# Optimization experiments

Measured on AMD Instinct MI355X. Metric: run time of the kernel, lower is better.

The kernel has to match this reference:

```python
import jax, jax.numpy as jnp
import numpy as np


def setup_inputs() -> dict:
    key = jax.random.key(0)
    k1, k2 = jax.random.split(key)
    B, D, H, W, K = 16, 256, 32, 32, 8192
    x = jax.random.normal(k1, (B, D, H, W), dtype=jnp.float32)
    # init_tensor: uniform [0,1), L2-normalized along dim 0 (embedding_dim), * embedding_scale
    e = jax.random.uniform(k2, (D, K), dtype=jnp.float32)
    e_i_ts = e / jnp.linalg.norm(e, axis=0, keepdims=True)
    return {"x": x, "e_i_ts": e_i_ts}


def reference(x, e_i_ts):
    B, D = x.shape[0], x.shape[1]
    spatial = x.shape[2:]
    # permute [B, D, *spatial] -> [B, *spatial, D], flatten tokens
    perm = (0,) + tuple(range(2, x.ndim)) + (1,)
    flat_x = jnp.transpose(x, perm).reshape(-1, D)  # [N, D]
    distances = (
        jnp.sum(flat_x * flat_x, axis=1, keepdims=True)
        - 2.0 * (flat_x @ e_i_ts)
        + jnp.sum(e_i_ts * e_i_ts, axis=0, keepdims=True)
    )
    encoding_indices = jnp.argmin(distances, axis=1)  # [N]
    ind = encoding_indices.reshape((B,) + spatial)  # [B, *spatial]
    # gather codebook columns: e_i_ts.T[ind] -> [B, *spatial, D], back to channel-first
    quantized = jnp.take(e_i_ts.T, ind, axis=0)
    inv_perm = (0, x.ndim - 1) + tuple(range(1, x.ndim - 1))
    quantized_x = jnp.transpose(quantized, inv_perm)  # [B, D, *spatial]
    # straight-through estimator
    quantized_x_d = x + jax.lax.stop_gradient(quantized_x - x)
    return quantized_x_d, quantized_x, ind
```

## Files before the change

kernel.cpp:

```cpp
#include <hip/hip_runtime.h>
#include <hip/hip_bf16.h>
#include <hip/hip_fp16.h>


#define D_   256
#define HW_  1024
#define N_   16384
#define K_   8192
#define NB_  32
#define MARGIN 0.02f

#define OUT1_OFF 4194304
#define IND_OFF  8388608

typedef __attribute__((ext_vector_type(8))) _Float16 f16x8;
typedef __attribute__((ext_vector_type(4))) float f32x4;

__device__ __forceinline__ unsigned long long pack_dk(float dist, int k) {
    unsigned db = __float_as_uint(dist);
    unsigned mono = (db & 0x80000000u) ? ~db : (db | 0x80000000u);
    return ((unsigned long long)mono << 32) | (unsigned)k;
}

__device__ __forceinline__ void async_copy16(const void* g, void* l) {
    __builtin_amdgcn_global_load_lds(
        (const __attribute__((address_space(1))) void*)g,
        (__attribute__((address_space(3))) void*)l, 16, 0, 0);
}

__global__ __launch_bounds__(256)
void cnorm_kernel(const float* __restrict__ E, float* __restrict__ c,
                  int* __restrict__ counters) {
    if (blockIdx.x == 0 && threadIdx.x < 2) counters[threadIdx.x] = 0;
    __shared__ float part[8][32];
    const int tid = threadIdx.x;
    const int cl = tid & 31, q = tid >> 5;
    const int k = blockIdx.x * 32 + cl;
    float s = 0.f;
    #pragma unroll 8
    for (int d = q * 32; d < q * 32 + 32; ++d) {
        float v = E[(size_t)d * K_ + k];
        s = fmaf(v, v, s);
    }
    part[q][cl] = s;
    __syncthreads();
    if (tid < 32) {
        float t0 = (part[0][tid] + part[1][tid]) + (part[2][tid] + part[3][tid]);
        float t1 = (part[4][tid] + part[5][tid]) + (part[6][tid] + part[7][tid]);
        c[blockIdx.x * 32 + tid] = t0 + t1;
    }
}

__global__ __launch_bounds__(256)
void prep_x(const float* __restrict__ x, ushort* __restrict__ xf) {
    __shared__ float t[32][33];
    const int s0 = blockIdx.x * 32, d0 = blockIdx.y * 32, b = blockIdx.z;
    const int tid = threadIdx.x;
    #pragma unroll
    for (int j = 0; j < 4; ++j) {
        int i = tid + 256 * j; int dd = i >> 5, ss = i & 31;
        t[dd][ss] = x[(size_t)b * 262144 + (size_t)(d0 + dd) * 1024 + s0 + ss];
    }
    __syncthreads();
    #pragma unroll
    for (int j = 0; j < 4; ++j) {
        int i = tid + 256 * j; int ss = i >> 5, dd = i & 31;
        _Float16 h = (_Float16)t[dd][ss];
        size_t o = (size_t)(b * 1024 + s0 + ss) * D_ + d0 + dd;
        xf[o] = *(ushort*)&h;
    }
}

__global__ __launch_bounds__(256)
void prep_e(const float* __restrict__ E, ushort* __restrict__ ef) {
    __shared__ float t[32][33];
    const int k0 = blockIdx.x * 32, d0 = blockIdx.y * 32;
    const int tid = threadIdx.x;
    #pragma unroll
    for (int j = 0; j < 4; ++j) {
        int i = tid + 256 * j; int dd = i >> 5, kk = i & 31;
        t[dd][kk] = E[(size_t)(d0 + dd) * K_ + k0 + kk];
    }
    __syncthreads();
    #pragma unroll
    for (int j = 0; j < 4; ++j) {
        int i = tid + 256 * j; int kk = i >> 5, dd = i & 31;
        _Float16 h = (_Float16)t[dd][kk];
        ef[(size_t)(k0 + kk) * D_ + d0 + dd] = *(ushort*)&h;
    }
}

__global__ __launch_bounds__(256, 3)
void mfma_kernel(const ushort* __restrict__ xf,
                 const ushort* __restrict__ ef,
                 const float* __restrict__ c,
                 float* __restrict__ pd1, int* __restrict__ pi1, float* __restrict__ pd2) {
    __shared__ __align__(16) ushort Ah[2][2048];
    __shared__ __align__(16) ushort Bb[2][8192];
    __shared__ unsigned red1[320], red2[320];

    const int tid = threadIdx.x;
    const int bid = blockIdx.x;
    const int xcd = bid & 7, rr = bid >> 3;
    const int nb = rr >> 5, mb = xcd * 32 + (rr & 31);
    const int n0 = mb * 64, k0 = nb * 256;
    const int lane = tid & 63, w = tid >> 6;
    const int l15 = lane & 15, lq = lane >> 4;

    size_t aoff;
    {
        int slot = w * 64 + lane;
        int t = slot >> 2, cp = slot & 3;
        int cs = cp ^ ((t >> 1) & 3);
        aoff = (size_t)(n0 + t) * D_ + cs * 8;
    }
    const int adst = w * 512;
    size_t boff[4]; int bdst[4];
    #pragma unroll
    for (int g = 0; g < 4; ++g) {
        int slot = (w * 4 + g) * 64 + lane;
        int t = slot >> 2, cp = slot & 3;
        int cs = cp ^ ((t >> 1) & 3);
        boff[g] = (size_t)(k0 + t) * D_ + cs * 8;
        bdst[g] = (w * 4 + g) * 512;
    }
    int aro[4], bro[4];
    #pragma unroll
    for (int mt = 0; mt < 4; ++mt) {
        int R = mt * 16 + l15;
        aro[mt] = R * 32 + ((lq ^ ((R >> 1) & 3)) * 8);
    }
    #pragma unroll
    for (int nt = 0; nt < 4; ++nt) {
        int R = w * 64 + nt * 16 + l15;
        bro[nt] = R * 32 + ((lq ^ ((R >> 1) & 3)) * 8);
    }

    f32x4 acc[4][4];
    #pragma unroll
    for (int mt = 0; mt < 4; ++mt)
        #pragma unroll
        for (int nt = 0; nt < 4; ++nt) acc[mt][nt] = (f32x4){0.f, 0.f, 0.f, 0.f};

    async_copy16(xf + aoff, &Ah[0][adst]);
    #pragma unroll
    for (int g = 0; g < 4; ++g)
        async_copy16(ef + boff[g], &Bb[0][bdst[g]]);
    __syncthreads();

    #pragma unroll
    for (int db = 0; db < 8; ++db) {
        const int cur = db & 1;
        const int d0 = db * 32;
        if (db < 7) {
            const int dn = d0 + 32;
            async_copy16(xf + aoff + dn, &Ah[cur ^ 1][adst]);
            #pragma unroll
            for (int g = 0; g < 4; ++g)
                async_copy16(ef + boff[g] + dn, &Bb[cur ^ 1][bdst[g]]);
        }
        f16x8 a[4], b[4];
        #pragma unroll
        for (int mt = 0; mt < 4; ++mt)
            a[mt] = *(const f16x8*)&Ah[cur][aro[mt]];
        #pragma unroll
        for (int nt = 0; nt < 4; ++nt)
            b[nt] = *(const f16x8*)&Bb[cur][bro[nt]];
        #pragma unroll
        for (int nt = 0; nt < 4; ++nt)
            #pragma unroll
            for (int mt = 0; mt < 4; ++mt)
                acc[mt][nt] = __builtin_amdgcn_mfma_f32_16x16x32_f16(a[mt], b[nt], acc[mt][nt], 0, 0, 0);
        __syncthreads();
    }

    float cv[4];
    #pragma unroll
    for (int nt = 0; nt < 4; ++nt) cv[nt] = c[k0 + w * 64 + nt * 16 + l15];

    unsigned m1[16], m2[16];
    #pragma unroll
    for (int mt = 0; mt < 4; ++mt)
        #pragma unroll
        for (int r = 0; r < 4; ++r) {
            int p = mt * 4 + r;
            unsigned b1 = 0xFFFFFFFFu, b2v = 0xFFFFFFFFu;
            #pragma unroll
            for (int nt = 0; nt < 4; ++nt) {
                float dist = fmaf(-2.f, acc[mt][nt][r], cv[nt]);
                unsigned u = (unsigned)fmaf(dist, 32768.f, 4194304.f);
                unsigned key = (u << 8) | (unsigned)(w * 64 + nt * 16 + l15);
                unsigned t = key > b1 ? key : b1;
                b1 = key < b1 ? key : b1;
                b2v = t < b2v ? t : b2v;
            }
            m1[p] = b1; m2[p] = b2v;
        }
    #pragma unroll
    for (int s = 1; s < 16; s <<= 1) {
        #pragma unroll
        for (int p = 0; p < 16; ++p) {
            unsigned n1 = (unsigned)__shfl_xor((int)m1[p], s);
            unsigned n2 = (unsigned)__shfl_xor((int)m2[p], s);
            unsigned t = m1[p] > n1 ? m1[p] : n1;
            m1[p] = m1[p] < n1 ? m1[p] : n1;
            unsigned mn = n2 < t ? n2 : t;
            m2[p] = m2[p] < mn ? m2[p] : mn;
        }
    }
    if (l15 == 0) {
        #pragma unroll
        for (int mt = 0; mt < 4; ++mt)
            #pragma unroll
            for (int r = 0; r < 4; ++r) {
                int p = mt * 4 + r;
                int t = mt * 16 + lq * 4 + r;
                red1[t * 5 + w] = m1[p]; red2[t * 5 + w] = m2[p];
            }
    }
    __syncthreads();
    if (tid < 64) {
        unsigned a1 = red1[tid * 5], a2v = red2[tid * 5];
        #pragma unroll
        for (int q = 1; q < 4; ++q) {
            unsigned n1 = red1[tid * 5 + q], n2 = red2[tid * 5 + q];
            unsigned t = a1 > n1 ? a1 : n1;
            a1 = a1 < n1 ? a1 : n1;
            unsigned mn = n2 < t ? n2 : t;
            a2v = a2v < mn ? a2v : mn;
        }
        size_t o = (size_t)nb * N_ + n0 + tid;
        pd1[o] = (float)(a1 >> 8) * (1.f / 32768.f) - 128.f;
        pi1[o] = k0 + (int)(a1 & 255u);
        pd2[o] = (float)(a2v >> 8) * (1.f / 32768.f) - 128.f;
    }
}

__global__ __launch_bounds__(256)
void merge_flag(const float* __restrict__ pd1, const int* __restrict__ pi1,
                const float* __restrict__ pd2,
                int* __restrict__ idx, int* __restrict__ counters,
                unsigned long long* __restrict__ key,
                unsigned int* __restrict__ pairs, unsigned int* __restrict__ scans) {
    int n = blockIdx.x * 256 + threadIdx.x;
    float a = 3.4e38f, b2 = 3.4e38f; int ai = -1;
    for (int nb = 0; nb < NB_; ++nb) {
        float n1 = pd1[(size_t)nb * N_ + n];
        int   ni = pi1[(size_t)nb * N_ + n];
        float n2 = pd2[(size_t)nb * N_ + n];
        if (n1 < a) { b2 = fminf(a, n2); a = n1; ai = ni; }
        else        { b2 = fminf(b2, n1); }
    }
    if (b2 - a < MARGIN) {
        const float W = a + MARGIN;
        key[n] = ~0ULL;
        idx[n] = 0x80000000 | ai;
        for (int nb = 0; nb < NB_; ++nb) {
            if (pd2[(size_t)nb * N_ + n] <= W) {
                int q = atomicAdd(&counters[1], 1);
                scans[q] = ((unsigned)n << 5) | (unsigned)nb;
            } else if (pd1[(size_t)nb * N_ + n] <= W) {
                int q = atomicAdd(&counters[0], 1);
                pairs[q] = ((unsigned)n << 13) | (unsigned)pi1[(size_t)nb * N_ + n];
            }
        }
    } else {
        idx[n] = ai;
    }
}

__global__ __launch_bounds__(256)
void recheck(const float* __restrict__ x, const float* __restrict__ E,
             const float* __restrict__ c, const unsigned int* __restrict__ pairs,
             const unsigned int* __restrict__ scans, const int* __restrict__ counters,
             unsigned long long* __restrict__ key) {
    if (blockIdx.x < 128) {
        int items = counters[0] * 4;
        for (int it = blockIdx.x * 256 + threadIdx.x; it < items; it += 128 * 256) {
            int p = it >> 2, q = it & 3;
            unsigned v = pairs[p];
            int n = v >> 13, k = v & 8191;
            int b = n >> 10, s = n & 1023;
            const float* xb = x + (size_t)b * 262144 + s;
            const float* eb = E + k;
            float acc = 0.f;
            const int d0 = q * 64;
            #pragma unroll 8
            for (int d = d0; d < d0 + 64; ++d)
                acc = fmaf(xb[(size_t)d * HW_], eb[(size_t)d * K_], acc);
            float o1 = __shfl_xor(acc, 1); float s2 = acc + o1;
            float o2 = __shfl_xor(s2, 2);  float tot = s2 + o2;
            if (q == 0) atomicMin(key + n, pack_dk(fmaf(-2.f, tot, c[k]), k));
        }
    } else {
        int cnt = counters[1];
        for (int t = blockIdx.x - 128; t < cnt; t += 256) {
            unsigned v = scans[t];
            int n = v >> 5, nb = v & 31;
            int k = nb * 256 + threadIdx.x;
            int b = n >> 10, s = n & 1023;
            const float* xb = x + (size_t)b * 262144 + s;
            float acc = 0.f;
            #pragma unroll 4
            for (int d = 0; d < D_; ++d)
                acc = fmaf(xb[(size_t)d * HW_], E[(size_t)d * K_ + k], acc);
            float dist = fmaf(-2.f, acc, c[k]);
            atomicMin(key + n, pack_dk(dist, k));
        }
    }
}

__global__ __launch_bounds__(256)
void write_kernel(const float* __restrict__ x, const float* __restrict__ E,
                  const int* __restrict__ idx, const unsigned long long* __restrict__ key,
                  float* __restrict__ out) {
    __shared__ int kst[64];
    const int n0 = blockIdx.x * 64;
    const int b = n0 >> 10, s0 = n0 & 1023;
    const int tid = threadIdx.x;
    if (tid < 64) {
        int v = idx[n0 + tid];
        int k = (v < 0) ? (int)(key[n0 + tid] & 8191ULL) : v;
        kst[tid] = k;
        if (blockIdx.y == 0) out[IND_OFF + n0 + tid] = (float)k;
    }
    __syncthreads();
    const int g = tid & 15;
    const int d0 = tid >> 4;
    const int dband = blockIdx.y * 64;
    const int ka = kst[g * 4], kb2 = kst[g * 4 + 1], kc = kst[g * 4 + 2], kd = kst[g * 4 + 3];
    const float* xb = x + (size_t)b * 262144 + s0 + g * 4;
    float* o0 = out + (size_t)b * 262144 + s0 + g * 4;
    float* o1 = o0 + OUT1_OFF;
    for (int d = dband + d0; d < dband + 64; d += 16) {
        const float* er = E + (size_t)d * K_;
        float4 xv = *(const float4*)(xb + (size_t)d * HW_);
        float4 q;
        q.x = er[ka]; q.y = er[kb2]; q.z = er[kc]; q.w = er[kd];
        float4 r;
        r.x = xv.x + (q.x - xv.x); r.y = xv.y + (q.y - xv.y);
        r.z = xv.z + (q.z - xv.z); r.w = xv.w + (q.w - xv.w);
        *(float4*)(o0 + (size_t)d * HW_) = r;
        *(float4*)(o1 + (size_t)d * HW_) = q;
    }
}

extern "C" void kernel_launch(void* const* d_in, const int* in_sizes, int n_in,
                              void* d_out, int out_size, void* d_ws, size_t ws_size,
                              hipStream_t stream) {
    const float* x = (const float*)d_in[0];
    const float* E = (const float*)d_in[1];
    float* out = (float*)d_out;

    char* p = (char*)d_ws;
    ushort* xf = (ushort*)p;                 p += (size_t)N_ * D_ * 2;
    ushort* ef = (ushort*)p;                 p += (size_t)K_ * D_ * 2;
    float*  c  = (float*)p;                  p += (size_t)K_ * 4;
    float*  pd1 = (float*)p;                 p += (size_t)NB_ * N_ * 4;
    int*    pi1 = (int*)p;                   p += (size_t)NB_ * N_ * 4;
    float*  pd2 = (float*)p;                 p += (size_t)NB_ * N_ * 4;
    int*    idx = (int*)p;                   p += (size_t)N_ * 4;
    unsigned long long* key = (unsigned long long*)p; p += (size_t)N_ * 8;
    unsigned int* pairs = (unsigned int*)p;  p += (size_t)524288 * 4;
    unsigned int* scans = (unsigned int*)p;  p += (size_t)524288 * 4;
    int*    counters = (int*)p;              p += 256;

    cnorm_kernel<<<K_ / 32, 256, 0, stream>>>(E, c, counters);
    prep_x<<<dim3(32, 8, 16), 256, 0, stream>>>(x, xf);
    prep_e<<<dim3(256, 8), 256, 0, stream>>>(E, ef);
    mfma_kernel<<<8192, 256, 0, stream>>>(xf, ef, c, pd1, pi1, pd2);
    merge_flag<<<N_ / 256, 256, 0, stream>>>(pd1, pi1, pd2, idx, counters, key, pairs, scans);
    recheck<<<384, 256, 0, stream>>>(x, E, c, pairs, scans, counters, key);
    write_kernel<<<dim3(256, 4), 256, 0, stream>>>(x, E, idx, key, out);
}
```

Before: 324.3 us.

## Enlarge MFMA block tile to 128x256 with 2x2 wave layout

Doubles the per-block token tile from 64 to 128 rows and arranges the four waves as a 2x2 grid. Each wave now computes a 64x128 sub-tile with 32 accumulators, so every loaded B fragment is reused across more MFMAs and the codebook is read from global memory half as often. The cost is a doubled accumulator register footprint and more LDS, which may lower occupancy below the launch-bounds target of three blocks. The cross-wave argmin reduction shrinks to a two-way merge.

```diff
diff --git a/kernel.cpp b/kernel.cpp
--- a/kernel.cpp
+++ b/kernel.cpp
@@ -95,26 +95,28 @@
                  const ushort* __restrict__ ef,
                  const float* __restrict__ c,
                  float* __restrict__ pd1, int* __restrict__ pi1, float* __restrict__ pd2) {
-    __shared__ __align__(16) ushort Ah[2][2048];
-    __shared__ __align__(16) ushort Bb[2][8192];
-    __shared__ unsigned red1[320], red2[320];
+    __shared__ __align__(16) ushort Af[2][4096];
+    __shared__ __align__(16) ushort Bf[2][8192];
+    __shared__ unsigned red1[384], red2[384];
 
     const int tid = threadIdx.x;
     const int bid = blockIdx.x;
     const int xcd = bid & 7, rr = bid >> 3;
-    const int nb = rr >> 5, mb = xcd * 32 + (rr & 31);
-    const int n0 = mb * 64, k0 = nb * 256;
+    const int nb = rr >> 4, mb = xcd * 16 + (rr & 15);
+    const int n0 = mb * 128, k0 = nb * 256;
     const int lane = tid & 63, w = tid >> 6;
+    const int wy = w >> 1, wx = w & 1;
     const int l15 = lane & 15, lq = lane >> 4;
 
-    size_t aoff;
-    {
-        int slot = w * 64 + lane;
+    size_t aoff[2]; int adst[2];
+    #pragma unroll
+    for (int g = 0; g < 2; ++g) {
+        int slot = (w * 2 + g) * 64 + lane;
         int t = slot >> 2, cp = slot & 3;
         int cs = cp ^ ((t >> 1) & 3);
-        aoff = (size_t)(n0 + t) * D_ + cs * 8;
-    }
-    const int adst = w * 512;
+        aoff[g] = (size_t)(n0 + t) * D_ + cs * 8;
+        adst[g] = (w * 2 + g) * 512;
+    }
     size_t boff[4]; int bdst[4];
     #pragma unroll
     for (int g = 0; g < 4; ++g) {
@@ -124,28 +126,30 @@
         boff[g] = (size_t)(k0 + t) * D_ + cs * 8;
         bdst[g] = (w * 4 + g) * 512;
     }
-    int aro[4], bro[4];
+    int aro[4], bro[8];
     #pragma unroll
     for (int mt = 0; mt < 4; ++mt) {
-        int R = mt * 16 + l15;
+        int R = wy * 64 + mt * 16 + l15;
         aro[mt] = R * 32 + ((lq ^ ((R >> 1) & 3)) * 8);
     }
     #pragma unroll
-    for (int nt = 0; nt < 4; ++nt) {
-        int R = w * 64 + nt * 16 + l15;
+    for (int nt = 0; nt < 8; ++nt) {
+        int R = wx * 128 + nt * 16 + l15;
         bro[nt] = R * 32 + ((lq ^ ((R >> 1) & 3)) * 8);
     }
 
-    f32x4 acc[4][4];
+    f32x4 acc[4][8];
     #pragma unroll
     for (int mt = 0; mt < 4; ++mt)
         #pragma unroll
-        for (int nt = 0; nt < 4; ++nt) acc[mt][nt] = (f32x4){0.f, 0.f, 0.f, 0.f};
-
-    async_copy16(xf + aoff, &Ah[0][adst]);
+        for (int nt = 0; nt < 8; ++nt) acc[mt][nt] = (f32x4){0.f, 0.f, 0.f, 0.f};
+
+    #pragma unroll
+    for (int g = 0; g < 2; ++g)
+        async_copy16(xf + aoff[g], &Af[0][adst[g]]);
     #pragma unroll
     for (int g = 0; g < 4; ++g)
-        async_copy16(ef + boff[g], &Bb[0][bdst[g]]);
+        async_copy16(ef + boff[g], &Bf[0][bdst[g]]);
     __syncthreads();
 
     #pragma unroll
@@ -154,29 +158,30 @@
         const int d0 = db * 32;
         if (db < 7) {
             const int dn = d0 + 32;
-            async_copy16(xf + aoff + dn, &Ah[cur ^ 1][adst]);
+            #pragma unroll
+            for (int g = 0; g < 2; ++g)
+                async_copy16(xf + aoff[g] + dn, &Af[cur ^ 1][adst[g]]);
             #pragma unroll
             for (int g = 0; g < 4; ++g)
-                async_copy16(ef + boff[g] + dn, &Bb[cur ^ 1][bdst[g]]);
-        }
-        f16x8 a[4], b[4];
+                async_copy16(ef + boff[g] + dn, &Bf[cur ^ 1][bdst[g]]);
+        }
+        f16x8 a[4];
         #pragma unroll
         for (int mt = 0; mt < 4; ++mt)
-            a[mt] = *(const f16x8*)&Ah[cur][aro[mt]];
-        #pragma unroll
-        for (int nt = 0; nt < 4; ++nt)
-            b[nt] = *(const f16x8*)&Bb[cur][bro[nt]];
-        #pragma unroll
-        for (int nt = 0; nt < 4; ++nt)
+            a[mt] = *(const f16x8*)&Af[cur][aro[mt]];
+        #pragma unroll
+        for (int nt = 0; nt < 8; ++nt) {
+            f16x8 b = *(const f16x8*)&Bf[cur][bro[nt]];
             #pragma unroll
             for (int mt = 0; mt < 4; ++mt)
-                acc[mt][nt] = __builtin_amdgcn_mfma_f32_16x16x32_f16(a[mt], b[nt], acc[mt][nt], 0, 0, 0);
+                acc[mt][nt] = __builtin_amdgcn_mfma_f32_16x16x32_f16(a[mt], b, acc[mt][nt], 0, 0, 0);
+        }
         __syncthreads();
     }
 
-    float cv[4];
-    #pragma unroll
-    for (int nt = 0; nt < 4; ++nt) cv[nt] = c[k0 + w * 64 + nt * 16 + l15];
+    float cv[8];
+    #pragma unroll
+    for (int nt = 0; nt < 8; ++nt) cv[nt] = c[k0 + wx * 128 + nt * 16 + l15];
 
     unsigned m1[16], m2[16];
     #pragma unroll
@@ -186,10 +191,10 @@
             int p = mt * 4 + r;
             unsigned b1 = 0xFFFFFFFFu, b2v = 0xFFFFFFFFu;
             #pragma unroll
-            for (int nt = 0; nt < 4; ++nt) {
+            for (int nt = 0; nt < 8; ++nt) {
                 float dist = fmaf(-2.f, acc[mt][nt][r], cv[nt]);
                 unsigned u = (unsigned)fmaf(dist, 32768.f, 4194304.f);
-                unsigned key = (u << 8) | (unsigned)(w * 64 + nt * 16 + l15);
+                unsigned key = (u << 8) | (unsigned)(wx * 128 + nt * 16 + l15);
                 unsigned t = key > b1 ? key : b1;
                 b1 = key < b1 ? key : b1;
                 b2v = t < b2v ? t : b2v;
@@ -214,21 +219,18 @@
             #pragma unroll
             for (int r = 0; r < 4; ++r) {
                 int p = mt * 4 + r;
-                int t = mt * 16 + lq * 4 + r;
-                red1[t * 5 + w] = m1[p]; red2[t * 5 + w] = m2[p];
+                int t = wy * 64 + mt * 16 + lq * 4 + r;
+                red1[t * 3 + wx] = m1[p]; red2[t * 3 + wx] = m2[p];
             }
     }
     __syncthreads();
-    if (tid < 64) {
-        unsigned a1 = red1[tid * 5], a2v = red2[tid * 5];
-        #pragma unroll
-        for (int q = 1; q < 4; ++q) {
-            unsigned n1 = red1[tid * 5 + q], n2 = red2[tid * 5 + q];
-            unsigned t = a1 > n1 ? a1 : n1;
-            a1 = a1 < n1 ? a1 : n1;
-            unsigned mn = n2 < t ? n2 : t;
-            a2v = a2v < mn ? a2v : mn;
-        }
+    if (tid < 128) {
+        unsigned a1 = red1[tid * 3], a2v = red2[tid * 3];
+        unsigned n1 = red1[tid * 3 + 1], n2 = red2[tid * 3 + 1];
+        unsigned t = a1 > n1 ? a1 : n1;
+        a1 = a1 < n1 ? a1 : n1;
+        unsigned mn = n2 < t ? n2 : t;
+        a2v = a2v < mn ? a2v : mn;
         size_t o = (size_t)nb * N_ + n0 + tid;
         pd1[o] = (float)(a1 >> 8) * (1.f / 32768.f) - 128.f;
         pi1[o] = k0 + (int)(a1 & 255u);
@@ -368,7 +370,7 @@
     cnorm_kernel<<<K_ / 32, 256, 0, stream>>>(E, c, counters);
     prep_x<<<dim3(32, 8, 16), 256, 0, stream>>>(x, xf);
     prep_e<<<dim3(256, 8), 256, 0, stream>>>(E, ef);
-    mfma_kernel<<<8192, 256, 0, stream>>>(xf, ef, c, pd1, pi1, pd2);
+    mfma_kernel<<<4096, 256, 0, stream>>>(xf, ef, c, pd1, pi1, pd2);
     merge_flag<<<N_ / 256, 256, 0, stream>>>(pd1, pi1, pd2, idx, counters, key, pairs, scans);
     recheck<<<384, 256, 0, stream>>>(x, E, c, pairs, scans, counters, key);
     write_kernel<<<dim3(256, 4), 256, 0, stream>>>(x, E, idx, key, out);
```

New measurement: 353.8 us. 1.09x slower.
